# Optimization experiments

Measured on AMD Instinct MI355X. Metric: run time of the kernel, lower is better.

The kernel has to match this reference:

```python
import jax, jax.numpy as jnp
import numpy as np

K = 16          # neighbors per node
EPS = 1e-5      # BatchNorm eps
BN_SCALE = 1.0 / np.sqrt(1.0 + EPS)  # eval BN with running mean=0, var=1


def _knn_idx(x, k):
    # x: [B, N, d] -> idx [B, N, k] of k nearest neighbors (self excluded)
    sq = jnp.sum(x * x, axis=-1)                               # [B, N]
    d2 = sq[:, :, None] + sq[:, None, :] - 2.0 * jnp.einsum('bnd,bmd->bnm', x, x)
    n = x.shape[1]
    d2 = jnp.where(jnp.eye(n, dtype=bool)[None], jnp.inf, d2)  # no self loops
    _, idx = jax.lax.top_k(-d2, k)
    return idx


def _edge_conv(x, idx, W, b, g, be):
    # PyG EdgeConv: max_j MLP([x_i, x_j - x_i]); MLP = Linear+BN(eval)+ReLU
    xj = jax.vmap(lambda xb, ib: xb[ib])(x, idx)               # [B, N, k, d]
    xi = x[:, :, None, :]
    m = jnp.concatenate([jnp.broadcast_to(xi, xj.shape), xj - xi], axis=-1)
    h = m @ W + b                                              # [B, N, k, out]
    h = g * (h * BN_SCALE) + be                                # eval BatchNorm
    h = jax.nn.relu(h)
    return jnp.max(h, axis=2)                                  # scatter-max over k


def setup_inputs() -> dict:
    key = jax.random.key(0)
    ks = jax.random.split(key, 16)
    B, N, D, C = 128, 256, 6, 12

    def w(k_, shape, fan_in):
        return (jax.random.normal(k_, shape, jnp.float32) / np.sqrt(fan_in)).astype(jnp.float32)

    inp = {
        'x':   jax.random.normal(ks[0], (B, N, D), jnp.float32),
        'W1':  w(ks[1], (2 * 6, 64), 12),   'b1': jnp.zeros((64,), jnp.float32),
        'g1':  jnp.ones((64,), jnp.float32), 'be1': jnp.zeros((64,), jnp.float32),
        'W2':  w(ks[2], (2 * 64, 128), 128), 'b2': jnp.zeros((128,), jnp.float32),
        'g2':  jnp.ones((128,), jnp.float32), 'be2': jnp.zeros((128,), jnp.float32),
        'W3':  w(ks[3], (2 * 128, 256), 256), 'b3': jnp.zeros((256,), jnp.float32),
        'g3':  jnp.ones((256,), jnp.float32), 'be3': jnp.zeros((256,), jnp.float32),
        'Wf1': w(ks[4], (256, 128), 256),    'bf1': jnp.zeros((128,), jnp.float32),
        'gf':  jnp.ones((128,), jnp.float32), 'bef': jnp.zeros((128,), jnp.float32),
        'Wf2': w(ks[5], (128, C), 128),      'bf2': jnp.zeros((C,), jnp.float32),
    }
    return inp


def reference(x, W1, b1, g1, be1, W2, b2, g2, be2, W3, b3, g3, be3,
              Wf1, bf1, gf, bef, Wf2, bf2):
    h = _edge_conv(x, _knn_idx(x, K), W1, b1, g1, be1)   # [B, N, 64]
    h = _edge_conv(h, _knn_idx(h, K), W2, b2, g2, be2)   # [B, N, 128]
    h = _edge_conv(h, _knn_idx(h, K), W3, b3, g3, be3)   # [B, N, 256]
    p = jnp.max(h, axis=1)                               # global_max_pool [B, 256]
    f = jax.nn.relu(gf * ((p @ Wf1 + bf1) * BN_SCALE) + bef)
    return f @ Wf2 + bf2                                 # [B, num_classes]
```

## Files before the change

### kernel.cpp

```cpp
#include <hip/hip_runtime.h>
#include <cstdint>
#include <cstddef>

#define KNN 16
#define NPTS 256
#define NBATCH 128

static constexpr float BN_SCALE_F = 0.9999950000374997f;

__device__ inline unsigned int f32_ord(float f) {
    unsigned int u = __float_as_uint(f);
    return (u & 0x80000000u) ? ~u : (u | 0x80000000u);
}

__device__ __forceinline__ int wmap(int n) { return n + 4 * (n >> 4); }

template<int D>
__global__ __launch_bounds__(256) void sq_kernel(const float* __restrict__ x,
                                                 float* __restrict__ sq) {
    const int t = blockIdx.x * 256 + threadIdx.x;
    const float* r = x + (size_t)t * D;
    float s = 0.f;
    #pragma unroll
    for (int d = 0; d < D; ++d) s = fmaf(r[d], r[d], s);
    sq[t] = s;
}

template<int D>
__global__ __launch_bounds__(256) void knn_fused_kernel(
        const float* __restrict__ x, const float* __restrict__ sq,
        int* __restrict__ idx) {
    constexpr int KS = (D >= 16) ? 16 : D;
    constexpr int NSTEP = D / KS;
    constexpr int NLOADG = (128 * KS + 255) / 256;
    const int t  = threadIdx.x;
    const int tx = t & 15, ty = t >> 4;
    const int sr = t >> 1, sc = t & 1;
    const int b  = blockIdx.x >> 1;
    const int i0 = (blockIdx.x & 1) * 128;
    const int base = b * NPTS;

    __shared__ float As[2][KS][132];
    __shared__ float Bs[2][KS][132];
    __shared__ float d2L[128][132];
    __shared__ unsigned char Mi[128][36];

    float4 pa[2], pb[2];
    float  pas[NLOADG], pbs[NLOADG];
    if constexpr (D % 16 == 0) {
        #pragma unroll
        for (int u = 0; u < 2; ++u) {
            const int e = t + u * 256, r = e >> 2, cq = (e & 3) * 4;
            pa[u] = *(const float4*)(x + (size_t)(base + i0 + r) * D + cq);
            pb[u] = *(const float4*)(x + (size_t)(base + r) * D + cq);
        }
    } else {
        #pragma unroll
        for (int u = 0; u < NLOADG; ++u) {
            const int e = t + u * 256;
            if (e < 128 * KS) {
                const int r = e / KS, c = e % KS;
                pas[u] = x[(size_t)(base + i0 + r) * D + c];
                pbs[u] = x[(size_t)(base + r) * D + c];
            }
        }
    }

    float sqi[8];
    #pragma unroll
    for (int m = 0; m < 8; ++m) sqi[m] = sq[base + i0 + ty * 8 + m];

    unsigned int Lv[16], Li[16];
    #pragma unroll
    for (int q = 0; q < 16; ++q) { Lv[q] = 0xFFFFFFFFu; Li[q] = 0u; }

    for (int jt = 0; jt < 2; ++jt) {
        const int j0 = jt * 128;
        float acc[8][8] = {};
        for (int s = 0; s < NSTEP; ++s) {
            const int g   = jt * NSTEP + s;
            const int buf = g & 1;
            if constexpr (D % 16 == 0) {
                #pragma unroll
                for (int u = 0; u < 2; ++u) {
                    const int e = t + u * 256, r = e >> 2, cq = (e & 3) * 4;
                    As[buf][cq + 0][r] = pa[u].x; As[buf][cq + 1][r] = pa[u].y;
                    As[buf][cq + 2][r] = pa[u].z; As[buf][cq + 3][r] = pa[u].w;
                    Bs[buf][cq + 0][r] = pb[u].x; Bs[buf][cq + 1][r] = pb[u].y;
                    Bs[buf][cq + 2][r] = pb[u].z; Bs[buf][cq + 3][r] = pb[u].w;
                }
            } else {
                #pragma unroll
                for (int u = 0; u < NLOADG; ++u) {
                    const int e = t + u * 256;
                    if (e < 128 * KS) {
                        const int r = e / KS, c = e % KS;
                        As[buf][c][r] = pas[u];
                        Bs[buf][c][r] = pbs[u];
                    }
                }
            }

            {
                const int gn2 = g + 1;
                const int njt = gn2 / NSTEP, ns = gn2 % NSTEP;
                if (njt < 2) {
                    if constexpr (D % 16 == 0) {
                        #pragma unroll
                        for (int u = 0; u < 2; ++u) {
                            const int e = t + u * 256, r = e >> 2, cq = (e & 3) * 4;
                            pa[u] = *(const float4*)(x + (size_t)(base + i0 + r) * D
                                                     + ns * KS + cq);
                            pb[u] = *(const float4*)(x + (size_t)(base + njt * 128 + r) * D
                                                     + ns * KS + cq);
                        }
                    } else {
                        #pragma unroll
                        for (int u = 0; u < NLOADG; ++u) {
                            const int e = t + u * 256;
                            if (e < 128 * KS) {
                                const int r = e / KS, c = e % KS;
                                pas[u] = x[(size_t)(base + i0 + r) * D + c];
                                pbs[u] = x[(size_t)(base + njt * 128 + r) * D + c];
                            }
                        }
                    }
                }
            }

            __syncthreads();

            #pragma unroll
            for (int kk = 0; kk < KS; ++kk) {
                float am[8], bm[8];
                *(float4*)&am[0] = *(const float4*)&As[buf][kk][ty * 8];
                *(float4*)&am[4] = *(const float4*)&As[buf][kk][ty * 8 + 4];
                *(float4*)&bm[0] = *(const float4*)&Bs[buf][kk][tx * 4];
                *(float4*)&bm[4] = *(const float4*)&Bs[buf][kk][64 + tx * 4];
                #pragma unroll
                for (int m = 0; m < 8; ++m)
                    #pragma unroll
                    for (int n = 0; n < 8; ++n)
                        acc[m][n] = fmaf(am[m], bm[n], acc[m][n]);
            }
        }

        float sqj[8];
        #pragma unroll
        for (int n = 0; n < 4; ++n) {
            sqj[n]     = sq[base + j0 + tx * 4 + n];
            sqj[n + 4] = sq[base + j0 + 64 + tx * 4 + n];
        }
        #pragma unroll
        for (int m = 0; m < 8; ++m) {
            const int gi = i0 + ty * 8 + m;
            float o0[4], o1[4];
            #pragma unroll
            for (int n = 0; n < 4; ++n) {
                float v0 = (sqi[m] + sqj[n])     - 2.f * acc[m][n];
                float v1 = (sqi[m] + sqj[n + 4]) - 2.f * acc[m][n + 4];
                if (gi == j0 + tx * 4 + n)      v0 = INFINITY;
                if (gi == j0 + 64 + tx * 4 + n) v1 = INFINITY;
                o0[n] = v0; o1[n] = v1;
            }
            *(float4*)&d2L[ty * 8 + m][tx * 4]      = make_float4(o0[0], o0[1], o0[2], o0[3]);
            *(float4*)&d2L[ty * 8 + m][64 + tx * 4] = make_float4(o1[0], o1[1], o1[2], o1[3]);
        }
        __syncthreads();

        #pragma unroll 4
        for (int i = 0; i < 64; ++i) {
            const unsigned int v = f32_ord(d2L[sr][sc * 64 + i]);
            const unsigned int j = (unsigned int)(j0 + sc * 64 + i);
            #pragma unroll
            for (int q = 15; q >= 1; --q) {
                const bool a = v < Lv[q];
                const bool c = v < Lv[q - 1];
                Lv[q] = a ? (c ? Lv[q - 1] : v) : Lv[q];
                Li[q] = a ? (c ? Li[q - 1] : j) : Li[q];
            }
            const bool a0 = v < Lv[0];
            Lv[0] = a0 ? v : Lv[0];
            Li[0] = a0 ? j : Li[0];
        }
    }

    __syncthreads();
    #pragma unroll
    for (int q = 0; q < 16; ++q) {
        d2L[sr][sc * 16 + q] = __uint_as_float(Lv[q]);
        Mi[sr][sc * 16 + q]  = (unsigned char)Li[q];
    }
    __syncthreads();

    if (t < 128) {
        const int row = t;
        int h[2];
        unsigned int cv[2], ci[2];
        #pragma unroll
        for (int c = 0; c < 2; ++c) {
            h[c]  = 0;
            cv[c] = __float_as_uint(d2L[row][c * 16]);
            ci[c] = Mi[row][c * 16];
        }
        int outj[16];
        #pragma unroll
        for (int rd = 0; rd < 16; ++rd) {
            const bool tk = (cv[1] < cv[0]) | ((cv[1] == cv[0]) & (ci[1] < ci[0]));
            const int bc = tk ? 1 : 0;
            outj[rd] = (int)(tk ? ci[1] : ci[0]);
            #pragma unroll
            for (int c = 0; c < 2; ++c) {
                if (c == bc) {
                    const int hn = h[c] + 1;
                    h[c] = hn;
                    if (hn < 16) {
                        cv[c] = __float_as_uint(d2L[row][c * 16 + hn]);
                        ci[c] = Mi[row][c * 16 + hn];
                    } else {
                        cv[c] = 0xFFFFFFFFu;
                    }
                }
            }
        }
        int4* op = (int4*)(idx + (size_t)(base + i0 + row) * KNN);
        op[0] = make_int4(outj[0],  outj[1],  outj[2],  outj[3]);
        op[1] = make_int4(outj[4],  outj[5],  outj[6],  outj[7]);
        op[2] = make_int4(outj[8],  outj[9],  outj[10], outj[11]);
        op[3] = make_int4(outj[12], outj[13], outj[14], outj[15]);
    }
}

template<int D, int C>
__global__ __launch_bounds__(256) void mlp_gemm_kernel(
        const float* __restrict__ x, const float* __restrict__ W,
        const float* __restrict__ bias, const float* __restrict__ g,
        const float* __restrict__ be,
        float* __restrict__ A, float* __restrict__ Bv) {
    constexpr int BM = 128;
    constexpr int KT = (D >= 16) ? 16 : D;
    constexpr int NSTEP = D / KT;
    constexpr int NXG = (BM * KT + 255) / 256;
    constexpr int NWG = (KT * 128 + 255) / 256;
    const int t  = threadIdx.x;
    const int tx = t & 15;
    const int ty = t >> 4;
    const int m0 = blockIdx.x * BM;
    const int n0 = blockIdx.y * 128;

    __shared__ float Xs[2][KT][132];
    __shared__ float Ws[2][KT][164];

    float acc[8][8] = {};

    const int xr = t >> 1, xc = (t & 1) * 8;
    const int wk = t >> 4, nq = (t & 15) * 8;
    const int gn = n0 + nq;
    const bool isTop = (gn < C);
    const int wcol = isTop ? gn : (gn - C);
    const int mb = wmap(nq);

    float4 px0, px1;
    float4 wt0, wt1, wb0, wb1;
    float  pxg[NXG], pwg[NWG];

    if constexpr (D % 16 == 0) {
        const float* xp = x + (size_t)(m0 + xr) * D + xc;
        px0 = *(const float4*)(xp);
        px1 = *(const float4*)(xp + 4);
        const float* pT = W + (size_t)wk * C + wcol;
        const float* pB = W + (size_t)(D + wk) * C + wcol;
        wt0 = *(const float4*)(pT); wt1 = *(const float4*)(pT + 4);
        wb0 = *(const float4*)(pB); wb1 = *(const float4*)(pB + 4);
    } else {
        #pragma unroll
        for (int u = 0; u < NXG; ++u) {
            const int e = t + u * 256;
            if (e < BM * KT) {
                const int r = e / KT, c = e % KT;
                pxg[u] = x[(size_t)(m0 + r) * D + c];
            }
        }
        #pragma unroll
        for (int u = 0; u < NWG; ++u) {
            const int e = t + u * 256;
            if (e < KT * 128) {
                const int k = e >> 7, n = e & 127;
                const int g2 = n0 + n;
                pwg[u] = (g2 < C)
                    ? W[(size_t)k * C + g2] - W[(size_t)(D + k) * C + g2]
                    : W[(size_t)(D + k) * C + (g2 - C)];
            }
        }
    }

    for (int s = 0; s < NSTEP; ++s) {
        const int buf = s & 1;
        if constexpr (D % 16 == 0) {
            Xs[buf][xc + 0][xr] = px0.x; Xs[buf][xc + 1][xr] = px0.y;
            Xs[buf][xc + 2][xr] = px0.z; Xs[buf][xc + 3][xr] = px0.w;
            Xs[buf][xc + 4][xr] = px1.x; Xs[buf][xc + 5][xr] = px1.y;
            Xs[buf][xc + 6][xr] = px1.z; Xs[buf][xc + 7][xr] = px1.w;
            float4 v0, v1;
            if (isTop) {
                v0 = make_float4(wt0.x - wb0.x, wt0.y - wb0.y,
                                 wt0.z - wb0.z, wt0.w - wb0.w);
                v1 = make_float4(wt1.x - wb1.x, wt1.y - wb1.y,
                                 wt1.z - wb1.z, wt1.w - wb1.w);
            } else {
                v0 = wb0; v1 = wb1;
            }
            *(float4*)&Ws[buf][wk][mb]     = v0;
            *(float4*)&Ws[buf][wk][mb + 4] = v1;
        } else {
            #pragma unroll
            for (int u = 0; u < NXG; ++u) {
                const int e = t + u * 256;
                if (e < BM * KT) {
                    const int r = e / KT, c = e % KT;
                    Xs[buf][c][r] = pxg[u];
                }
            }
            #pragma unroll
            for (int u = 0; u < NWG; ++u) {
                const int e = t + u * 256;
                if (e < KT * 128) {
                    const int k = e >> 7, n = e & 127;
                    Ws[buf][k][wmap(n)] = pwg[u];
                }
            }
        }

        if (s + 1 < NSTEP) {
            const int k0n = (s + 1) * KT;
            if constexpr (D % 16 == 0) {
                const float* xp = x + (size_t)(m0 + xr) * D + k0n + xc;
                px0 = *(const float4*)(xp);
                px1 = *(const float4*)(xp + 4);
                const float* pT = W + (size_t)(k0n + wk) * C + wcol;
                const float* pB = W + (size_t)(D + k0n + wk) * C + wcol;
                wt0 = *(const float4*)(pT); wt1 = *(const float4*)(pT + 4);
                wb0 = *(const float4*)(pB); wb1 = *(const float4*)(pB + 4);
            } else {
                #pragma unroll
                for (int u = 0; u < NXG; ++u) {
                    const int e = t + u * 256;
                    if (e < BM * KT) {
                        const int r = e / KT, c = e % KT;
                        pxg[u] = x[(size_t)(m0 + r) * D + k0n + c];
                    }
                }
                #pragma unroll
                for (int u = 0; u < NWG; ++u) {
                    const int e = t + u * 256;
                    if (e < KT * 128) {
                        const int k = e >> 7, n = e & 127;
                        const int g2 = n0 + n;
                        pwg[u] = (g2 < C)
                            ? W[(size_t)(k0n + k) * C + g2] - W[(size_t)(D + k0n + k) * C + g2]
                            : W[(size_t)(D + k0n + k) * C + (g2 - C)];
                    }
                }
            }
        }

        __syncthreads();

        const int mc = wmap(tx * 8);
        #pragma unroll
        for (int kk = 0; kk < KT; ++kk) {
            float xm[8], wn[8];
            *(float4*)&xm[0] = *(const float4*)&Xs[buf][kk][ty * 8];
            *(float4*)&xm[4] = *(const float4*)&Xs[buf][kk][ty * 8 + 4];
            *(float4*)&wn[0] = *(const float4*)&Ws[buf][kk][mc];
            *(float4*)&wn[4] = *(const float4*)&Ws[buf][kk][mc + 4];
            #pragma unroll
            for (int m = 0; m < 8; ++m)
                #pragma unroll
                for (int n = 0; n < 8; ++n)
                    acc[m][n] = fmaf(xm[m], wn[n], acc[m][n]);
        }
    }

    if (isTop) {
        float fac[8];
        #pragma unroll
        for (int e = 0; e < 8; ++e) fac[e] = g[gn + e] * BN_SCALE_F;
        #pragma unroll
        for (int m = 0; m < 8; ++m) {
            float o[8];
            #pragma unroll
            for (int e = 0; e < 8; ++e) o[e] = fac[e] * acc[m][e];
            float* dst = A + (size_t)(m0 + ty * 8 + m) * C + gn;
            *(float4*)(dst)     = make_float4(o[0], o[1], o[2], o[3]);
            *(float4*)(dst + 4) = make_float4(o[4], o[5], o[6], o[7]);
        }
    } else {
        const int cb = gn - C;
        float fac[8], bb[8], bee[8];
        #pragma unroll
        for (int e = 0; e < 8; ++e) {
            fac[e] = g[cb + e] * BN_SCALE_F;
            bb[e]  = bias[cb + e];
            bee[e] = be[cb + e];
        }
        #pragma unroll
        for (int m = 0; m < 8; ++m) {
            float o[8];
            #pragma unroll
            for (int e = 0; e < 8; ++e)
                o[e] = fmaf(fac[e], acc[m][e] + bb[e], bee[e]);
            float* dst = Bv + (size_t)(m0 + ty * 8 + m) * C + cb;
            *(float4*)(dst)     = make_float4(o[0], o[1], o[2], o[3]);
            *(float4*)(dst + 4) = make_float4(o[4], o[5], o[6], o[7]);
        }
    }
}

template<int C>
__global__ __launch_bounds__(C) void combine_kernel(
        const float* A, const float* __restrict__ Bv,
        const int* __restrict__ idx, float* out) {
    const int bi = blockIdx.x;
    const int c  = threadIdx.x;
    __shared__ int nbr[KNN];
    if (c < KNN) nbr[c] = idx[(size_t)bi * KNN + c];
    __syncthreads();
    const int b0 = bi & ~255;
    float mx = -INFINITY;
    #pragma unroll
    for (int kk = 0; kk < KNN; ++kk)
        mx = fmaxf(mx, Bv[(size_t)(b0 + nbr[kk]) * C + c]);
    float a = A[(size_t)bi * C + c];
    out[(size_t)bi * C + c] = fmaxf(a + mx, 0.f);
}

__global__ __launch_bounds__(256) void head_kernel(
        const float* __restrict__ h3, const float* __restrict__ Wf1,
        const float* __restrict__ bf1, const float* __restrict__ gf,
        const float* __restrict__ bef, const float* __restrict__ Wf2,
        const float* __restrict__ bf2, float* __restrict__ out) {
    const int b   = blockIdx.x;
    const int tid = threadIdx.x;
    __shared__ float p[256];
    __shared__ float f[128];
    const float* hb = h3 + (size_t)b * NPTS * 256;
    float mx = -INFINITY;
    for (int n = 0; n < NPTS; ++n) mx = fmaxf(mx, hb[(size_t)n * 256 + tid]);
    p[tid] = mx;
    __syncthreads();
    if (tid < 128) {
        float acc = bf1[tid];
        for (int d = 0; d < 256; ++d)
            acc = fmaf(p[d], Wf1[(size_t)d * 128 + tid], acc);
        float v = gf[tid] * (acc * BN_SCALE_F) + bef[tid];
        f[tid] = fmaxf(v, 0.f);
    }
    __syncthreads();
    if (tid < 12) {
        float acc = bf2[tid];
        for (int d = 0; d < 128; ++d)
            acc = fmaf(f[d], Wf2[(size_t)d * 12 + tid], acc);
        out[(size_t)b * 12 + tid] = acc;
    }
}

extern "C" void kernel_launch(void* const* d_in, const int* in_sizes, int n_in,
                              void* d_out, int out_size, void* d_ws, size_t ws_size,
                              hipStream_t stream) {
    const float* x   = (const float*)d_in[0];
    const float* W1  = (const float*)d_in[1];
    const float* b1  = (const float*)d_in[2];
    const float* g1  = (const float*)d_in[3];
    const float* be1 = (const float*)d_in[4];
    const float* W2  = (const float*)d_in[5];
    const float* b2  = (const float*)d_in[6];
    const float* g2  = (const float*)d_in[7];
    const float* be2 = (const float*)d_in[8];
    const float* W3  = (const float*)d_in[9];
    const float* b3  = (const float*)d_in[10];
    const float* g3  = (const float*)d_in[11];
    const float* be3 = (const float*)d_in[12];
    const float* Wf1 = (const float*)d_in[13];
    const float* bf1 = (const float*)d_in[14];
    const float* gf  = (const float*)d_in[15];
    const float* bef = (const float*)d_in[16];
    const float* Wf2 = (const float*)d_in[17];
    const float* bf2 = (const float*)d_in[18];
    float* out = (float*)d_out;

    char* ws = (char*)d_ws;
    const size_t idx_bytes = (size_t)NBATCH * NPTS * KNN * sizeof(int);
    const size_t reg_bytes = (size_t)NBATCH * NPTS * 256 * sizeof(float);
    int*   idx = (int*)ws;
    float* R1  = (float*)(ws + idx_bytes);
    float* R2  = (float*)(ws + idx_bytes + reg_bytes);
    float* R3  = (float*)(ws + idx_bytes + 2 * reg_bytes);
    float* sqb = (float*)(ws + idx_bytes + 3 * reg_bytes);

    const int BN = NBATCH * NPTS;
    const int KNN_GRID = NBATCH * 2;
    const int MB = BN / 128;

    sq_kernel<6><<<BN / 256, 256, 0, stream>>>(x, sqb);
    knn_fused_kernel<6><<<KNN_GRID, 256, 0, stream>>>(x, sqb, idx);
    mlp_gemm_kernel<6, 64><<<dim3(MB, 1), 256, 0, stream>>>(
        x, W1, b1, g1, be1, R1, R2);
    combine_kernel<64><<<BN, 64, 0, stream>>>(R1, R2, idx, R1);

    sq_kernel<64><<<BN / 256, 256, 0, stream>>>(R1, sqb);
    knn_fused_kernel<64><<<KNN_GRID, 256, 0, stream>>>(R1, sqb, idx);
    mlp_gemm_kernel<64, 128><<<dim3(MB, 2), 256, 0, stream>>>(
        R1, W2, b2, g2, be2, R2, R3);
    combine_kernel<128><<<BN, 128, 0, stream>>>(R2, R3, idx, R2);

    sq_kernel<128><<<BN / 256, 256, 0, stream>>>(R2, sqb);
    knn_fused_kernel<128><<<KNN_GRID, 256, 0, stream>>>(R2, sqb, idx);
    mlp_gemm_kernel<128, 256><<<dim3(MB, 4), 256, 0, stream>>>(
        R2, W3, b3, g3, be3, R3, R1);
    combine_kernel<256><<<BN, 256, 0, stream>>>(R3, R1, idx, R3);

    head_kernel<<<NBATCH, 256, 0, stream>>>(R3, Wf1, bf1, gf, bef, Wf2, bf2, out);
}
```

Baseline: 460.1 us.

## Split kNN into 64-row blocks sharing one staged point tile

```diff
diff --git a/kernel.cpp b/kernel.cpp
--- a/kernel.cpp
+++ b/kernel.cpp
@@ -32,146 +32,135 @@
         int* __restrict__ idx) {
     constexpr int KS = (D >= 16) ? 16 : D;
     constexpr int NSTEP = D / KS;
-    constexpr int NLOADG = (128 * KS + 255) / 256;
+    constexpr int NLOADG = (256 * KS + 255) / 256;
     const int t  = threadIdx.x;
     const int tx = t & 15, ty = t >> 4;
-    const int sr = t >> 1, sc = t & 1;
-    const int b  = blockIdx.x >> 1;
-    const int i0 = (blockIdx.x & 1) * 128;
+    const int srow = t >> 2, sch = t & 3;
+    const int b  = blockIdx.x >> 2;
+    const int i0 = (blockIdx.x & 3) * 64;
     const int base = b * NPTS;
 
-    __shared__ float As[2][KS][132];
-    __shared__ float Bs[2][KS][132];
-    __shared__ float d2L[128][132];
-    __shared__ unsigned char Mi[128][36];
-
-    float4 pa[2], pb[2];
-    float  pas[NLOADG], pbs[NLOADG];
+    __shared__ float Bs[2][KS][260];
+    __shared__ float d2L[64][132];
+    __shared__ unsigned char Mi[64][68];
+
+    float4 pb[4];
+    float  pbs[NLOADG];
     if constexpr (D % 16 == 0) {
         #pragma unroll
-        for (int u = 0; u < 2; ++u) {
+        for (int u = 0; u < 4; ++u) {
             const int e = t + u * 256, r = e >> 2, cq = (e & 3) * 4;
-            pa[u] = *(const float4*)(x + (size_t)(base + i0 + r) * D + cq);
             pb[u] = *(const float4*)(x + (size_t)(base + r) * D + cq);
         }
     } else {
         #pragma unroll
         for (int u = 0; u < NLOADG; ++u) {
             const int e = t + u * 256;
-            if (e < 128 * KS) {
+            if (e < 256 * KS) {
                 const int r = e / KS, c = e % KS;
-                pas[u] = x[(size_t)(base + i0 + r) * D + c];
                 pbs[u] = x[(size_t)(base + r) * D + c];
             }
         }
     }
 
-    float sqi[8];
+    float sqi[4];
     #pragma unroll
-    for (int m = 0; m < 8; ++m) sqi[m] = sq[base + i0 + ty * 8 + m];
-
-    unsigned int Lv[16], Li[16];
-    #pragma unroll
-    for (int q = 0; q < 16; ++q) { Lv[q] = 0xFFFFFFFFu; Li[q] = 0u; }
-
-    for (int jt = 0; jt < 2; ++jt) {
-        const int j0 = jt * 128;
-        float acc[8][8] = {};
-        for (int s = 0; s < NSTEP; ++s) {
-            const int g   = jt * NSTEP + s;
-            const int buf = g & 1;
+    for (int m = 0; m < 4; ++m) sqi[m] = sq[base + i0 + ty * 4 + m];
+
+    float acc[4][16] = {};
+
+    for (int s = 0; s < NSTEP; ++s) {
+        const int buf = s & 1;
+        if constexpr (D % 16 == 0) {
+            #pragma unroll
+            for (int u = 0; u < 4; ++u) {
+                const int e = t + u * 256, r = e >> 2, cq = (e & 3) * 4;
+                Bs[buf][cq + 0][r] = pb[u].x; Bs[buf][cq + 1][r] = pb[u].y;
+                Bs[buf][cq + 2][r] = pb[u].z; Bs[buf][cq + 3][r] = pb[u].w;
+            }
+        } else {
+            #pragma unroll
+            for (int u = 0; u < NLOADG; ++u) {
+                const int e = t + u * 256;
+                if (e < 256 * KS) {
+                    const int r = e / KS, c = e % KS;
+                    Bs[buf][c][r] = pbs[u];
+                }
+            }
+        }
+
+        if (s + 1 < NSTEP) {
+            const int k0n = (s + 1) * KS;
             if constexpr (D % 16 == 0) {
                 #pragma unroll
-                for (int u = 0; u < 2; ++u) {
+                for (int u = 0; u < 4; ++u) {
                     const int e = t + u * 256, r = e >> 2, cq = (e & 3) * 4;
-                    As[buf][cq + 0][r] = pa[u].x; As[buf][cq + 1][r] = pa[u].y;
-                    As[buf][cq + 2][r] = pa[u].z; As[buf][cq + 3][r] = pa[u].w;
-                    Bs[buf][cq + 0][r] = pb[u].x; Bs[buf][cq + 1][r] = pb[u].y;
-                    Bs[buf][cq + 2][r] = pb[u].z; Bs[buf][cq + 3][r] = pb[u].w;
+                    pb[u] = *(const float4*)(x + (size_t)(base + r) * D + k0n + cq);
                 }
             } else {
                 #pragma unroll
                 for (int u = 0; u < NLOADG; ++u) {
                     const int e = t + u * 256;
-                    if (e < 128 * KS) {
+                    if (e < 256 * KS) {
                         const int r = e / KS, c = e % KS;
-                        As[buf][c][r] = pas[u];
-                        Bs[buf][c][r] = pbs[u];
+                        pbs[u] = x[(size_t)(base + r) * D + k0n + c];
                     }
                 }
             }
-
-            {
-                const int gn2 = g + 1;
-                const int njt = gn2 / NSTEP, ns = gn2 % NSTEP;
-                if (njt < 2) {
-                    if constexpr (D % 16 == 0) {
-                        #pragma unroll
-                        for (int u = 0; u < 2; ++u) {
-                            const int e = t + u * 256, r = e >> 2, cq = (e & 3) * 4;
-                            pa[u] = *(const float4*)(x + (size_t)(base + i0 + r) * D
-                                                     + ns * KS + cq);
-                            pb[u] = *(const float4*)(x + (size_t)(base + njt * 128 + r) * D
-                                                     + ns * KS + cq);
-                        }
-                    } else {
-                        #pragma unroll
-                        for (int u = 0; u < NLOADG; ++u) {
-                            const int e = t + u * 256;
-                            if (e < 128 * KS) {
-                                const int r = e / KS, c = e % KS;
-                                pas[u] = x[(size_t)(base + i0 + r) * D + c];
-                                pbs[u] = x[(size_t)(base + njt * 128 + r) * D + c];
-                            }
-                        }
-                    }
-                }
-            }
-
-            __syncthreads();
-
-            #pragma unroll
-            for (int kk = 0; kk < KS; ++kk) {
-                float am[8], bm[8];
-                *(float4*)&am[0] = *(const float4*)&As[buf][kk][ty * 8];
-                *(float4*)&am[4] = *(const float4*)&As[buf][kk][ty * 8 + 4];
-                *(float4*)&bm[0] = *(const float4*)&Bs[buf][kk][tx * 4];
-                *(float4*)&bm[4] = *(const float4*)&Bs[buf][kk][64 + tx * 4];
+        }
+
+        __syncthreads();
+
+        #pragma unroll
+        for (int kk = 0; kk < KS; ++kk) {
+            float am[4], bm[16];
+            *(float4*)&am[0] = *(const float4*)&Bs[buf][kk][i0 + ty * 4];
+            #pragma unroll
+            for (int q = 0; q < 4; ++q)
+                *(float4*)&bm[q * 4] = *(const float4*)&Bs[buf][kk][q * 64 + tx * 4];
+            #pragma unroll
+            for (int m = 0; m < 4; ++m)
                 #pragma unroll
-                for (int m = 0; m < 8; ++m)
-                    #pragma unroll
-                    for (int n = 0; n < 8; ++n)
-                        acc[m][n] = fmaf(am[m], bm[n], acc[m][n]);
-            }
-        }
+                for (int n = 0; n < 16; ++n)
+                    acc[m][n] = fmaf(am[m], bm[n], acc[m][n]);
+        }
+    }
+
+    unsigned int Lv[16], Li[16];
+    #pragma unroll
+    for (int q = 0; q < 16; ++q) { Lv[q] = 0xFFFFFFFFu; Li[q] = 0u; }
+
+    #pragma unroll
+    for (int ph = 0; ph < 2; ++ph) {
+        if (ph == 1) __syncthreads();
 
         float sqj[8];
         #pragma unroll
-        for (int n = 0; n < 4; ++n) {
-            sqj[n]     = sq[base + j0 + tx * 4 + n];
-            sqj[n + 4] = sq[base + j0 + 64 + tx * 4 + n];
-        }
-        #pragma unroll
-        for (int m = 0; m < 8; ++m) {
-            const int gi = i0 + ty * 8 + m;
+        for (int w = 0; w < 4; ++w) {
+            sqj[w]     = sq[base + ph * 128 + tx * 4 + w];
+            sqj[w + 4] = sq[base + ph * 128 + 64 + tx * 4 + w];
+        }
+        #pragma unroll
+        for (int m = 0; m < 4; ++m) {
+            const int gi = i0 + ty * 4 + m;
             float o0[4], o1[4];
             #pragma unroll
-            for (int n = 0; n < 4; ++n) {
-                float v0 = (sqi[m] + sqj[n])     - 2.f * acc[m][n];
-                float v1 = (sqi[m] + sqj[n + 4]) - 2.f * acc[m][n + 4];
-                if (gi == j0 + tx * 4 + n)      v0 = INFINITY;
-                if (gi == j0 + 64 + tx * 4 + n) v1 = INFINITY;
-                o0[n] = v0; o1[n] = v1;
-            }
-            *(float4*)&d2L[ty * 8 + m][tx * 4]      = make_float4(o0[0], o0[1], o0[2], o0[3]);
-            *(float4*)&d2L[ty * 8 + m][64 + tx * 4] = make_float4(o1[0], o1[1], o1[2], o1[3]);
+            for (int w = 0; w < 4; ++w) {
+                float v0 = (sqi[m] + sqj[w])     - 2.f * acc[m][8 * ph + w];
+                float v1 = (sqi[m] + sqj[w + 4]) - 2.f * acc[m][8 * ph + 4 + w];
+                if (gi == ph * 128 + tx * 4 + w)      v0 = INFINITY;
+                if (gi == ph * 128 + 64 + tx * 4 + w) v1 = INFINITY;
+                o0[w] = v0; o1[w] = v1;
+            }
+            *(float4*)&d2L[ty * 4 + m][tx * 4]      = make_float4(o0[0], o0[1], o0[2], o0[3]);
+            *(float4*)&d2L[ty * 4 + m][64 + tx * 4] = make_float4(o1[0], o1[1], o1[2], o1[3]);
         }
         __syncthreads();
 
         #pragma unroll 4
-        for (int i = 0; i < 64; ++i) {
-            const unsigned int v = f32_ord(d2L[sr][sc * 64 + i]);
-            const unsigned int j = (unsigned int)(j0 + sc * 64 + i);
+        for (int i = 0; i < 32; ++i) {
+            const unsigned int v = f32_ord(d2L[srow][sch + 4 * i]);
+            const unsigned int j = (unsigned int)(ph * 128 + sch + 4 * i);
             #pragma unroll
             for (int q = 15; q >= 1; --q) {
                 const bool a = v < Lv[q];
@@ -188,17 +177,17 @@
     __syncthreads();
     #pragma unroll
     for (int q = 0; q < 16; ++q) {
-        d2L[sr][sc * 16 + q] = __uint_as_float(Lv[q]);
-        Mi[sr][sc * 16 + q]  = (unsigned char)Li[q];
+        d2L[srow][sch * 16 + q] = __uint_as_float(Lv[q]);
+        Mi[srow][sch * 16 + q]  = (unsigned char)Li[q];
     }
     __syncthreads();
 
-    if (t < 128) {
+    if (t < 64) {
         const int row = t;
-        int h[2];
-        unsigned int cv[2], ci[2];
-        #pragma unroll
-        for (int c = 0; c < 2; ++c) {
+        int h[4];
+        unsigned int cv[4], ci[4];
+        #pragma unroll
+        for (int c = 0; c < 4; ++c) {
             h[c]  = 0;
             cv[c] = __float_as_uint(d2L[row][c * 16]);
             ci[c] = Mi[row][c * 16];
@@ -206,11 +195,18 @@
         int outj[16];
         #pragma unroll
         for (int rd = 0; rd < 16; ++rd) {
-            const bool tk = (cv[1] < cv[0]) | ((cv[1] == cv[0]) & (ci[1] < ci[0]));
-            const int bc = tk ? 1 : 0;
-            outj[rd] = (int)(tk ? ci[1] : ci[0]);
-            #pragma unroll
-            for (int c = 0; c < 2; ++c) {
+            unsigned int bv = cv[0], bi = ci[0];
+            int bc = 0;
+            #pragma unroll
+            for (int c = 1; c < 4; ++c) {
+                const bool tk = (cv[c] < bv) | ((cv[c] == bv) & (ci[c] < bi));
+                bv = tk ? cv[c] : bv;
+                bi = tk ? ci[c] : bi;
+                bc = tk ? c     : bc;
+            }
+            outj[rd] = (int)bi;
+            #pragma unroll
+            for (int c = 0; c < 4; ++c) {
                 if (c == bc) {
                     const int hn = h[c] + 1;
                     h[c] = hn;
@@ -499,7 +495,7 @@
     float* sqb = (float*)(ws + idx_bytes + 3 * reg_bytes);
 
     const int BN = NBATCH * NPTS;
-    const int KNN_GRID = NBATCH * 2;
+    const int KNN_GRID = NBATCH * 4;
     const int MB = BN / 128;
 
     sq_kernel<6><<<BN / 256, 256, 0, stream>>>(x, sqb);
```

After: 475.8 us. 3.4% more time.
